# Optimization experiments

Measured on AMD Instinct MI355X. Metric: run time of the kernel, lower is better.

## Reference

```python
import jax, jax.numpy as jnp
import numpy as np
from math import factorial, pi, sqrt

N_ATOMS = 4096
N_PAIRS = 49152
F = 16           # num_tensordense_features
NUM_RADIAL = 16  # basis num=16
NUM_SPECIES = 95
EMB_DIM = 32
CUTOFF = 5.0
LMAX = 4         # SelfAttention max_degree=4
NLM = 25
LMAX_B = 2       # basis max_degree=2 (also max_tensordense_degree)
NLM_B = 9

DEG9 = np.repeat(np.arange(3), [1, 3, 5])        # degree index of each lm, l<=2
DEG25 = np.repeat(np.arange(5), [1, 3, 5, 7, 9]) # degree index of each lm, l<=4


def real_sph(u, lmax):
    # real spherical harmonics (m = -l..l ordering, no Condon-Shortley), u: (...,3) unit vectors
    x, y, z = u[..., 0], u[..., 1], u[..., 2]
    phi = jnp.arctan2(y, x)
    ct = jnp.clip(z, -1.0, 1.0)
    st = jnp.sqrt(jnp.clip(1.0 - ct * ct, 0.0, 1.0))
    P = {(0, 0): jnp.ones_like(ct)}
    for m in range(1, lmax + 1):
        P[(m, m)] = -(2 * m - 1) * st * P[(m - 1, m - 1)]
    for m in range(0, lmax):
        P[(m + 1, m)] = (2 * m + 1) * ct * P[(m, m)]
    for m in range(0, lmax + 1):
        for l in range(m + 2, lmax + 1):
            P[(l, m)] = ((2 * l - 1) * ct * P[(l - 1, m)] - (l + m - 1) * P[(l - 2, m)]) / (l - m)
    outs = []
    for l in range(lmax + 1):
        for m in range(-l, l + 1):
            ma = abs(m)
            Nn = sqrt((2 * l + 1) / (4 * pi) * factorial(l - ma) / factorial(l + ma))
            cs = (-1.0) ** ma  # cancel Condon-Shortley in P
            if m == 0:
                Y = Nn * P[(l, 0)]
            elif m > 0:
                Y = sqrt(2.0) * Nn * cs * jnp.cos(m * phi) * P[(l, m)]
            else:
                Y = sqrt(2.0) * Nn * cs * jnp.sin(ma * phi) * P[(l, ma)]
            outs.append(Y)
    return jnp.stack(outs, axis=-1)


def _gaunt():
    # exact real Gaunt (CG-equivalent) coupling coefficients via Gauss-Legendre x uniform-phi quadrature
    nt, nph = 16, 32
    xs, ws = np.polynomial.legendre.leggauss(nt)
    phis = np.arange(nph) * (2 * np.pi / nph)
    ct = np.repeat(xs, nph); ph = np.tile(phis, nt)
    st = np.sqrt(np.clip(1.0 - ct ** 2, 0.0, 1.0))
    u = np.stack([st * np.cos(ph), st * np.sin(ph), ct], -1)
    w = np.repeat(ws, nph) * (2 * np.pi / nph)
    Y = np.asarray(real_sph(jnp.asarray(u, dtype=jnp.float32), LMAX))
    G = np.einsum('gi,gj,gk,g->ijk', Y, Y[:, :NLM_B], Y, w)
    G[np.abs(G) < 1e-6] = 0.0
    return G

_G = _gaunt()
G_ATT = jnp.asarray(_G, dtype=jnp.float32)                      # (25, 9, 25): feat x basis -> feat
G_TD = jnp.asarray(_G[:NLM_B, :, :NLM_B], dtype=jnp.float32)    # (9, 9, 9): TensorDense coupling


def pdense(x, W, deg):
    return jnp.einsum('plf,lfg->plg', x, W[deg])


def couple(xf, Bf, G):
    # equivariant tensor product  out[p,k,f] = sum_ij G[i,j,k] xf[p,i,f] Bf[p,j,f]
    u = jnp.einsum('pif,ijk->pjkf', xf, G)
    return jnp.einsum('pjf,pjkf->pkf', Bf, u)


def setup_inputs() -> dict:
    key = jax.random.key(0)
    ks = jax.random.split(key, 24)
    s = 1.0 / np.sqrt(F)
    inp = dict(
        atomic_numbers=jax.random.randint(ks[0], (N_ATOMS,), 0, NUM_SPECIES),
        neighbour_indices=jnp.stack([
            jax.random.randint(ks[1], (N_PAIRS,), 0, N_ATOMS),
            jax.random.randint(ks[2], (N_PAIRS,), 0, N_ATOMS)], axis=-1),
        neighbour_displacements=jax.random.normal(ks[3], (N_PAIRS, 3), dtype=jnp.float32) * 1.7,
        W_rad=jax.random.normal(ks[4], (NUM_SPECIES, NUM_RADIAL, F), dtype=jnp.float32) / np.sqrt(NUM_RADIAL),
        emb_table=jax.random.normal(ks[5], (NUM_SPECIES, EMB_DIM), dtype=jnp.float32),
        W_emb=jax.random.normal(ks[6], (EMB_DIM, F), dtype=jnp.float32) / np.sqrt(EMB_DIM),
        b_emb=jnp.zeros((F,), jnp.float32),
        td_W1=jax.random.normal(ks[7], (3, F, F), dtype=jnp.float32) * s,
        td_W2=jax.random.normal(ks[8], (3, F, F), dtype=jnp.float32) * s,
        td_W3=jax.random.normal(ks[9], (3, F, F), dtype=jnp.float32) * s,
        Wb1=jax.random.normal(ks[10], (NUM_RADIAL, F), dtype=jnp.float32) / np.sqrt(NUM_RADIAL),
        Wq1=jax.random.normal(ks[11], (5, F, F), dtype=jnp.float32) * s,
        Wk1=jax.random.normal(ks[12], (5, F, F), dtype=jnp.float32) * s,
        Wv1=jax.random.normal(ks[13], (5, F, F), dtype=jnp.float32) * s,
        Wo1=jax.random.normal(ks[14], (5, F, F), dtype=jnp.float32) * s,
        bo1=jnp.zeros((F,), jnp.float32),
        Wb2=jax.random.normal(ks[15], (NUM_RADIAL, F), dtype=jnp.float32) / np.sqrt(NUM_RADIAL),
        Wq2=jax.random.normal(ks[16], (5, F, F), dtype=jnp.float32) * s,
        Wk2=jax.random.normal(ks[17], (5, F, F), dtype=jnp.float32) * s,
        Wv2=jax.random.normal(ks[18], (5, F, F), dtype=jnp.float32) * s,
        Wo2=jax.random.normal(ks[19], (5, F, F), dtype=jnp.float32) * s,
        bo2=jnp.zeros((F,), jnp.float32),
    )
    return inp


def reference(atomic_numbers, neighbour_indices, neighbour_displacements,
              W_rad, emb_table, W_emb, b_emb, td_W1, td_W2, td_W3,
              Wb1, Wq1, Wk1, Wv1, Wo1, bo1, Wb2, Wq2, Wk2, Wv2, Wo2, bo2):
    dst = neighbour_indices[:, 0]   # idx_i
    src = neighbour_indices[:, 1]   # idx_j
    Zj = atomic_numbers[src]
    r = jnp.linalg.norm(neighbour_displacements, axis=-1)
    u = neighbour_displacements / jnp.maximum(r, 1e-9)[:, None]
    sh = real_sph(u, LMAX)          # (P, 25)
    sh_b = sh[:, :NLM_B]            # (P, 9)
    kk = jnp.arange(1, NUM_RADIAL + 1, dtype=jnp.float32)
    rb = jnp.sinc(kk[None, :] * r[:, None] / CUTOFF) * (r < CUTOFF)[:, None]  # sinc basis w/ cutoff
    # species-aware radial basis -> per-pair equivariant features (P, 9, F)
    y0 = jnp.einsum('pk,pkf->pf', rb, W_rad[Zj])
    y = sh_b[:, :, None] * y0[:, None, :]
    # TensorDense: dense -> CG tensor product -> dense (degrees <= 2)
    a = pdense(y, td_W1, DEG9)
    b = pdense(y, td_W2, DEG9)
    u9 = jnp.einsum('pif,ijk->pjkf', a, G_TD)
    tp = jnp.einsum('pjf,pjkf->pkf', b, u9)
    y = pdense(tp, td_W3, DEG9)
    # aggregate per-pair messages to atoms (segment mean), pad degrees to l<=4
    sums = jnp.zeros((N_ATOMS, NLM_B, F), y.dtype).at[dst].add(y)
    cnt = jnp.zeros((N_ATOMS,), y.dtype).at[dst].add(1.0)
    x = sums / jnp.maximum(cnt, 1.0)[:, None, None]
    x = jnp.pad(x, ((0, 0), (0, NLM - NLM_B), (0, 0)))  # (N, 25, F)
    # two segment self-attention layers over neighbour pairs
    for (Wb, Wq, Wk, Wv, Wo, bo) in ((Wb1, Wq1, Wk1, Wv1, Wo1, bo1), (Wb2, Wq2, Wk2, Wv2, Wo2, bo2)):
        Bf = sh_b[:, :, None] * (rb @ Wb)[:, None, :]   # projected pair basis (P, 9, F)
        q = pdense(x, Wq, DEG25)[dst]
        kf = couple(pdense(x, Wk, DEG25)[src], Bf, G_ATT)
        vf = couple(pdense(x, Wv, DEG25)[src], Bf, G_ATT)
        s = jnp.einsum('plf,plf->p', q, kf) / np.sqrt(NLM * F)
        m = jax.lax.stop_gradient(jnp.full((N_ATOMS,), -1e30, s.dtype).at[dst].max(s))
        e = jnp.exp(s - m[dst])
        den = jnp.zeros((N_ATOMS,), s.dtype).at[dst].add(e)
        alpha = e / (den[dst] + 1e-9)
        agg = jnp.zeros((N_ATOMS, NLM, F), x.dtype).at[dst].add(alpha[:, None, None] * vf)
        x = pdense(agg, Wo, DEG25)
        x = x.at[:, 0, :].add(bo)
    # embedding residual connection on the scalar (l=0) channel
    res = emb_table[atomic_numbers] @ W_emb + b_emb
    x = x.at[:, 0, :].add(res)
    return x
```

## Files before the change

### kernel.cpp

```cpp
#include <hip/hip_runtime.h>
#include <hip/hip_bf16.h>

#define NA 4096
#define NP 49152

typedef _Float16 f16;
typedef _Float16 h2 __attribute__((ext_vector_type(2)));
union U4H { uint4 u; f16 h[8]; h2 p[4]; };

__device__ __forceinline__ float fdot2(h2 a, h2 b, float c){
#if __has_builtin(__builtin_amdgcn_fdot2)
  return __builtin_amdgcn_fdot2(a, b, c, false);
#else
  return c + (float)a.x*(float)b.x + (float)a.y*(float)b.y;
#endif
}

constexpr int WS_AOFS9 = 64;
constexpr int WS_ATTW9 = 128;
constexpr int WS_ATTIJ9= WS_ATTW9 + 512;
constexpr int WS_G     = 12800;
constexpr int WS_NATT  = WS_G + 5632;
constexpr int WS_ATTW  = WS_NATT + 8;
constexpr int WS_ATTIJ = WS_ATTW + 1024;
constexpr int WS_TDOFS = WS_ATTIJ + 1024;
constexpr int WS_TDW   = WS_TDOFS + 16;
constexpr int WS_TDIJ  = WS_TDW + 512;
constexpr int WS_AOFS  = WS_TDIJ + 512;
constexpr int WS_SH    = WS_AOFS + 32;
constexpr int WS_RB    = WS_SH + NP*9;
constexpr int WS_S     = WS_RB + NP*16;
constexpr int WS_CCNT  = WS_S + NP;
constexpr int WS_COFF  = WS_CCNT + NA;
constexpr int WS_CCUR  = WS_COFF + NA + 8;
constexpr int WS_CLST  = WS_CCUR + NA;
constexpr int WS_XQ    = WS_CLST + NP;
constexpr int WS_XK    = WS_XQ + NA*400;
constexpr int WS_XV    = WS_XK + NA*400;
constexpr int WS_PVF   = WS_XV + NA*400;
constexpr int WS_WW    = WS_PVF + NP*128;
constexpr int WS_PVFE  = WS_PVF + NP*256;
constexpr int WS_INV   = WS_PVFE;
constexpr int WS_DS    = WS_INV + NP;
constexpr long long WS_END = (long long)WS_DS + 2*NP + 16;

__device__ const float  GLX[16] = {
  -0.98940093499164993f, -0.94457502307323258f, -0.86563120238783174f, -0.75540440835500303f,
  -0.61787624440264375f, -0.45801677765722739f, -0.28160355077925891f, -0.09501250983763744f,
   0.09501250983763744f,  0.28160355077925891f,  0.45801677765722739f,  0.61787624440264375f,
   0.75540440835500303f,  0.86563120238783174f,  0.94457502307323258f,  0.98940093499164993f };
__device__ const double GLW[16] = {
  0.02715245941175409, 0.06225352393864789, 0.09515851168249278, 0.12462897125553387,
  0.14959598881657673, 0.16915651939500254, 0.18260341504492359, 0.18945061045506850,
  0.18945061045506850, 0.18260341504492359, 0.16915651939500254, 0.14959598881657673,
  0.12462897125553387, 0.09515851168249278, 0.06225352393864789, 0.02715245941175409 };

#define PI_D 3.14159265358979323846

__device__ __forceinline__ float scrub(float v){
  if(!(v == v)) return 0.f;
  return fminf(fmaxf(v, -1e30f), 1e30f);
}

__device__ void real_sph25(float ct, float phi, float* Y){
  float st = sqrtf(fmaxf(0.f, 1.f - ct*ct));
  float P[5][5];
  P[0][0] = 1.f;
  #pragma unroll
  for(int m=1;m<=4;m++) P[m][m] = -(2.f*m - 1.f)*st*P[m-1][m-1];
  #pragma unroll
  for(int m=0;m<4;m++) P[m+1][m] = (2.f*m + 1.f)*ct*P[m][m];
  #pragma unroll
  for(int m=0;m<=4;m++){
    #pragma unroll
    for(int l=m+2;l<=4;l++)
      P[l][m] = ((2.f*l - 1.f)*ct*P[l-1][m] - (float)(l+m-1)*P[l-2][m]) / (float)(l-m);
  }
  const double fact[9] = {1,1,2,6,24,120,720,5040,40320};
  int idx = 0;
  #pragma unroll
  for(int l=0;l<=4;l++){
    #pragma unroll
    for(int m=-l;m<=l;m++){
      int ma = (m < 0) ? -m : m;
      float Nn = (float)sqrt((2*l+1)/(4.0*PI_D)*fact[l-ma]/fact[l+ma]);
      float cs = (ma & 1) ? -1.f : 1.f;
      float v;
      if(m == 0)      v = Nn * P[l][0];
      else if(m > 0)  v = 1.4142135623730951f * Nn * cs * cosf(ma*phi) * P[l][ma];
      else            v = 1.4142135623730951f * Nn * cs * sinf(ma*phi) * P[l][ma];
      Y[idx++] = v;
    }
  }
}

__global__ __launch_bounds__(256) void kq_G(float* ws){
  __shared__ float Ysh[12800];
  int tid = threadIdx.x;
  for(int pt=tid; pt<512; pt+=256){
    float ct  = GLX[pt >> 5];
    float phi = (float)((pt & 31) * (2.0*PI_D/32.0));
    float Y[25];
    real_sph25(ct, phi, Y);
    #pragma unroll
    for(int i=0;i<25;i++) Ysh[pt*25 + i] = Y[i];
  }
  __syncthreads();
  int idx = blockIdx.x*256 + tid;
  int t = idx >> 3, chunk = idx & 7;
  if(t >= 5625) return;
  int k = t % 25, j = (t/25) % 9, i = t/225;
  double acc = 0.0;
  int g0 = chunk*64;
  #pragma unroll 4
  for(int g=g0; g<g0+64; g++){
    double w = GLW[g >> 5] * (2.0*PI_D/32.0);
    acc += w * (double)Ysh[g*25+i] * (double)Ysh[g*25+j] * (double)Ysh[g*25+k];
  }
  acc += __shfl_xor(acc, 1, 8);
  acc += __shfl_xor(acc, 2, 8);
  acc += __shfl_xor(acc, 4, 8);
  if(chunk == 0){
    if(fabs(acc) < 1e-6) acc = 0.0;
    ws[WS_G + (i*9+j)*25 + k] = (float)acc;
  }
}

__global__ __launch_bounds__(64) void kq_lists(float* ws){
  __shared__ float Gsh[5632];
  __shared__ int cA[25], cT[9], cA9[25], oA[26], oT[10], oA9[26];
  int t = threadIdx.x;
  for(int i=t; i<5625; i+=64) Gsh[i] = ws[WS_G + i];
  __syncthreads();
  const float* G = Gsh;
  if(t < 25){
    int c=0, c9=0;
    for(int i=0;i<25;i++) for(int j=0;j<9;j++) if(G[(i*9+j)*25+t] != 0.f){ c++; if(i<9) c9++; }
    cA[t]=c; cA9[t]=c9;
  }
  if(t < 9){  int c=0; for(int i=0;i<9;i++)  for(int j=0;j<9;j++) if(G[(i*9+j)*25+t] != 0.f) c++; cT[t]=c; }
  __syncthreads();
  if(t == 0){
    int s=0; for(int k=0;k<25;k++){ oA[k]=s; s+=cA[k]; } oA[25]=s;
    ((int*)ws)[WS_NATT] = s;
    s=0; for(int k=0;k<25;k++){ oA9[k]=s; s+=cA9[k]; } oA9[25]=s;
    s=0; for(int k=0;k<9;k++){ oT[k]=s; s+=cT[k]; } oT[9]=s;
  }
  __syncthreads();
  float* attw = ws + WS_ATTW;  int* attij = (int*)ws + WS_ATTIJ;
  float* attw9 = ws + WS_ATTW9; int* attij9 = (int*)ws + WS_ATTIJ9;
  int* aofs  = (int*)ws + WS_AOFS;
  int* aofs9 = (int*)ws + WS_AOFS9;
  if(t < 26){ aofs[t] = oA[t] < 1024 ? oA[t] : 1024; aofs9[t] = oA9[t] < 512 ? oA9[t] : 512; }
  if(t < 25){
    int pos = oA[t], pos9 = oA9[t];
    for(int i=0;i<25;i++) for(int j=0;j<9;j++){
      float w = G[(i*9+j)*25+t];
      if(w != 0.f){
        if(pos < 1024){ attw[pos]=w; attij[pos] = i | (j<<5) | (t<<9); pos++; }
        if(i < 9 && pos9 < 512){ attw9[pos9]=w; attij9[pos9] = i | (j<<5) | (t<<9); pos9++; }
      }
    }
  }
  float* tdw = ws + WS_TDW; int* tdij = (int*)ws + WS_TDIJ; int* tdofs = (int*)ws + WS_TDOFS;
  if(t < 9){
    int pos = oT[t];
    for(int i=0;i<9;i++) for(int j=0;j<9;j++){
      float w = G[(i*9+j)*25+t];
      if(w != 0.f && pos < 512){
        int li = (i==0)?0:(i<4)?1:2, lj = (j==0)?0:(j<4)?1:2;
        tdw[pos]=w; tdij[pos] = i | (j<<5) | (li<<10) | (lj<<12); pos++;
      }
    }
    tdofs[t] = oT[t];
    if(t == 0) tdofs[9] = oT[9];
  }
}

__global__ void k_cnt(const int* nbr, float* ws){
  int p = blockIdx.x*256 + threadIdx.x;
  if(p >= NP) return;
  atomicAdd((int*)ws + WS_CCNT + nbr[2*p], 1);
}

__global__ __launch_bounds__(1024) void k_scan(float* ws){
  __shared__ int part[1024];
  int t = threadIdx.x;
  const int* cnt = (const int*)ws + WS_CCNT;
  int v0 = cnt[4*t], v1 = cnt[4*t+1], v2 = cnt[4*t+2], v3 = cnt[4*t+3];
  part[t] = v0+v1+v2+v3;
  __syncthreads();
  for(int o=1; o<1024; o<<=1){
    int x = (t >= o) ? part[t-o] : 0;
    __syncthreads();
    part[t] += x;
    __syncthreads();
  }
  int base = (t > 0) ? part[t-1] : 0;
  int* offp = (int*)ws + WS_COFF;
  int* cur  = (int*)ws + WS_CCUR;
  offp[4*t]   = base;          cur[4*t]   = base;
  offp[4*t+1] = base+v0;       cur[4*t+1] = base+v0;
  offp[4*t+2] = base+v0+v1;    cur[4*t+2] = base+v0+v1;
  offp[4*t+3] = base+v0+v1+v2; cur[4*t+3] = base+v0+v1+v2;
  if(t == 1023) offp[4096] = part[1023];
}

__global__ void k_fill(const int* nbr, float* ws){
  int p = blockIdx.x*256 + threadIdx.x;
  if(p >= NP) return;
  int d = nbr[2*p], s = nbr[2*p+1];
  int pos = atomicAdd((int*)ws + WS_CCUR + d, 1);
  ((int*)ws)[WS_CLST + pos] = p;
  ((int*)ws)[WS_INV + p] = pos;
  ((int*)ws)[WS_DS + 2*pos]     = d;
  ((int*)ws)[WS_DS + 2*pos + 1] = s;
}

__global__ void k_pair(const float* disp, float* ws){
  int p = blockIdx.x*256 + threadIdx.x;
  if(p >= NP) return;
  int sp = ((const int*)ws)[WS_INV + p];
  float dx = disp[3*p], dy = disp[3*p+1], dz = disp[3*p+2];
  float r = sqrtf(dx*dx + dy*dy + dz*dz);
  float inv = 1.f / fmaxf(r, 1e-9f);
  float ux = dx*inv, uy = dy*inv, uz = dz*inv;
  float sh[9];
  sh[0] = 0.28209479177387814f;
  sh[1] = 0.4886025119029199f * uy;
  sh[2] = 0.4886025119029199f * uz;
  sh[3] = 0.4886025119029199f * ux;
  sh[4] = 1.0925484305920792f * ux*uy;
  sh[5] = 1.0925484305920792f * uy*uz;
  sh[6] = 0.31539156525252005f * (3.f*uz*uz - 1.f);
  sh[7] = 1.0925484305920792f * ux*uz;
  sh[8] = 0.5462742152960396f * (ux*ux - uy*uy);
  #pragma unroll
  for(int i=0;i<9;i++) ws[WS_SH + sp*9 + i] = scrub(sh[i]);
  float mask = (r < 5.f) ? 1.f : 0.f;
  float rbv[16];
  #pragma unroll
  for(int k=1;k<=16;k++){
    float x  = (float)k * r * 0.2f;
    float px = 3.14159265358979323846f * x;
    float s  = (px < 1e-6f) ? 1.f : (sinf(px)/px);
    rbv[k-1] = scrub(s * mask);
  }
  float4* rb4 = (float4*)(ws + WS_RB + sp*16);
  #pragma unroll
  for(int c=0;c<4;c++) rb4[c] = make_float4(rbv[4*c], rbv[4*c+1], rbv[4*c+2], rbv[4*c+3]);
}

__global__ __launch_bounds__(256) void k_ww(const float* Wrad, const float* W1,
                                            const float* W2, float* ws){
  int s = blockIdx.x;
  #pragma unroll
  for(int it=0; it<6; it++){
    int idx = threadIdx.x + 256*it;
    int w = idx / 768, r = idx % 768;
    int d = r / 256, r2 = r % 256, k = r2 / 16, g = r2 % 16;
    const float* Wsrc = (w == 0) ? W1 : W2;
    float acc = 0.f;
    #pragma unroll
    for(int fp=0; fp<16; fp++)
      acc += Wrad[(s*16+k)*16+fp] * Wsrc[(d*16+fp)*16+g];
    ws[WS_WW + ((size_t)(s*2+w)*16 + g)*48 + d*16 + k] = acc;
  }
}

__global__ __launch_bounds__(256) void k_td(const int* aZ, const float* W3, float* ws){
  __shared__ float sh_s[16][9];
  __shared__ float S_s[16][88];
  __shared__ float tp_s[16][9][16];
  int tid = threadIdx.x, pl = tid >> 4, g = tid & 15;
  int sp = blockIdx.x*16 + pl;
  int src = ((const int*)ws)[WS_DS + 2*sp + 1];
  int Zj = aZ[src];
  {
    float4* S4 = (float4*)&S_s[0][0];
    for(int t0=tid; t0<352; t0+=256) S4[t0] = make_float4(0.f,0.f,0.f,0.f);
  }
  if(g < 9) sh_s[pl][g] = ws[WS_SH + sp*9 + g];
  float rb[16];
  {
    const float4* rb4 = (const float4*)(ws + WS_RB + sp*16);
    #pragma unroll
    for(int c=0;c<4;c++){
      float4 r = rb4[c];
      rb[4*c]=r.x; rb[4*c+1]=r.y; rb[4*c+2]=r.z; rb[4*c+3]=r.w;
    }
  }
  float A1[3], A2[3];
  {
    const float4* w1 = (const float4*)(ws + WS_WW + ((size_t)(Zj*2+0)*16+g)*48);
    const float4* w2 = (const float4*)(ws + WS_WW + ((size_t)(Zj*2+1)*16+g)*48);
    #pragma unroll
    for(int d=0; d<3; d++){
      float a1 = 0.f, a2 = 0.f;
      #pragma unroll
      for(int c=0;c<4;c++){
        float4 x1 = w1[d*4+c], x2 = w2[d*4+c];
        a1 += x1.x*rb[4*c] + x1.y*rb[4*c+1] + x1.z*rb[4*c+2] + x1.w*rb[4*c+3];
        a2 += x2.x*rb[4*c] + x2.y*rb[4*c+1] + x2.z*rb[4*c+2] + x2.w*rb[4*c+3];
      }
      A1[d] = a1; A2[d] = a2;
    }
  }
  __syncthreads();
  if(g < 9){
    const float* tdw = ws + WS_TDW;
    const int* tdij  = (const int*)ws + WS_TDIJ;
    const int* tdofs = (const int*)ws + WS_TDOFS;
    int e1 = tdofs[g+1];
    for(int e=tdofs[g]; e<e1; e++){
      float w = tdw[e]; int meta = tdij[e];
      int i = meta & 31, j = (meta>>5) & 15, li = (meta>>10) & 3, lj = (meta>>12) & 3;
      S_s[pl][g*9 + li*3 + lj] += w * sh_s[pl][i] * sh_s[pl][j];
    }
  }
  __syncthreads();
  float AA[9];
  #pragma unroll
  for(int li=0;li<3;li++)
    #pragma unroll
    for(int lj=0;lj<3;lj++) AA[li*3+lj] = A1[li]*A2[lj];
  #pragma unroll
  for(int k=0;k<9;k++){
    float tpv = 0.f;
    #pragma unroll
    for(int c=0;c<9;c++) tpv += S_s[pl][k*9+c] * AA[c];
    tp_s[pl][k][g] = tpv;
  }
  __syncthreads();
  float w3r[48];
  #pragma unroll
  for(int d=0;d<3;d++)
    #pragma unroll
    for(int f2=0;f2<16;f2++) w3r[d*16+f2] = W3[(d*16+f2)*16+g];
  float acc9[9];
  #pragma unroll
  for(int k=0;k<9;k++){
    int d = (k==0)?0:(k<4)?1:2;
    const float4* t4 = (const float4*)&tp_s[pl][k][0];
    float acc = 0.f;
    #pragma unroll
    for(int c=0;c<4;c++){
      float4 t = t4[c];
      acc += t.x*w3r[d*16+4*c] + t.y*w3r[d*16+4*c+1] + t.z*w3r[d*16+4*c+2] + t.w*w3r[d*16+4*c+3];
    }
    acc9[k] = scrub(acc);
  }
  f16* ptd = (f16*)(ws + WS_PVF) + (size_t)sp*256 + g*16;
  U4H u0, u1;
  #pragma unroll
  for(int j=0;j<8;j++) u0.h[j] = (f16)acc9[j];
  u1.h[0] = (f16)acc9[8];
  #pragma unroll
  for(int j=1;j<8;j++) u1.h[j] = (f16)0.f;
  *(uint4*)(ptd)     = u0.u;
  *(uint4*)(ptd + 8) = u1.u;
}

__global__ __launch_bounds__(256) void k_tdq(const float* Wq, const float* Wk,
                                             const float* Wv, float* ws){
  __shared__ float xsh[4][144];
  __shared__ float wq_sh[768], wk_sh[768], wv_sh[768];
  int tid = threadIdx.x, al = tid >> 6, lane = tid & 63;
  int a = blockIdx.x*4 + al;
  for(int t=tid; t<768; t+=256){ wq_sh[t]=Wq[t]; wk_sh[t]=Wk[t]; wv_sh[t]=Wv[t]; }
  const int* coff = (const int*)ws + WS_COFF;
  int off0 = coff[a], n = coff[a+1] - off0;
  const f16* base = (const f16*)(ws + WS_PVF);
  float acc[8] = {0,0,0,0,0,0,0,0};
  if(lane < 32){
    for(int t=0; t<n; t++){
      U4H u; u.u = *(const uint4*)(base + (size_t)(off0+t)*256 + lane*8);
      #pragma unroll
      for(int j=0;j<8;j++) acc[j] += (float)u.h[j];
    }
  }
  float invn = 1.f / fmaxf((float)n, 1.f);
  if(lane < 32){
    int gg = lane >> 1;
    #pragma unroll
    for(int j=0;j<8;j++){
      int k = (lane & 1)*8 + j;
      if(k < 9) xsh[al][k*16 + gg] = scrub(acc[j]*invn);
    }
  }
  __syncthreads();
  int g = lane & 15, q4 = lane >> 4;
  f16* qt = (f16*)(ws + WS_XQ) + (size_t)a*800 + g*32;
  f16* kt = (f16*)(ws + WS_XK) + (size_t)a*800 + g*32;
  f16* vt = (f16*)(ws + WS_XV) + (size_t)a*800 + g*32;
  for(int i=q4; i<9; i+=4){
    int l = (i==0)?0:(i<4)?1:2;
    float q=0.f, k2=0.f, v2=0.f;
    #pragma unroll
    for(int f2=0;f2<16;f2++){
      float xv = xsh[al][i*16+f2];
      q  += xv*wq_sh[(l*16+f2)*16+g];
      k2 += xv*wk_sh[(l*16+f2)*16+g];
      v2 += xv*wv_sh[(l*16+f2)*16+g];
    }
    qt[i] = (f16)q; kt[i] = (f16)k2; vt[i] = (f16)v2;
  }
}

template<int NI>
__global__ __launch_bounds__(128) void k_att(const float* Wb, float* ws){
  constexpr int MROWH = (NI == 9) ? 16 : 32;
  constexpr int PLSTR = (NI == 9) ? 408 : 840;
  __shared__ __align__(16) f16 Ml[8][PLSTR];
  __shared__ float sh_s[8][9];
  __shared__ float wb_sh[256];
  constexpr int NPAIR = NI/2;
  constexpr int TAIL  = NI-1;
  int tid = threadIdx.x, pl = tid >> 4, g = tid & 15;
  int sp = blockIdx.x*8 + pl;
  {
    uint4 z; z.x=0; z.y=0; z.z=0; z.w=0;
    uint4* Mz = (uint4*)&Ml[0][0];
    for(int t0=tid; t0<PLSTR; t0+=128) Mz[t0] = z;
  }
  for(int t0=tid; t0<256; t0+=128) wb_sh[t0] = Wb[t0];
  if(g < 9) sh_s[pl][g] = ws[WS_SH + sp*9 + g];
  __syncthreads();
  {
    const float* attw = ws + (NI==9 ? WS_ATTW9 : WS_ATTW);
    const int* attij  = (const int*)ws + (NI==9 ? WS_ATTIJ9 : WS_ATTIJ);
    const int* aofs   = (const int*)ws + (NI==9 ? WS_AOFS9 : WS_AOFS);
    for(int kr=g; kr<25; kr+=16){
      f16* Mrow = &Ml[pl][kr*MROWH];
      int e = aofs[kr], e1 = aofs[kr+1];
      if(e < e1){
        int meta = attij[e];
        int curi = meta & 31;
        float cur = 0.f;
        for(; e<e1; e++){
          meta = attij[e];
          int i2 = meta & 31;
          if(i2 != curi){ Mrow[curi] = (f16)cur; cur = 0.f; curi = i2; }
          cur += attw[e] * sh_s[pl][(meta>>5) & 15];
        }
        Mrow[curi] = (f16)cur;
      }
    }
  }
  __syncthreads();
  int dst = ((const int*)ws)[WS_DS + 2*sp];
  int src = ((const int*)ws)[WS_DS + 2*sp + 1];
  float q_r[NI];
  {
    const f16* qt = (const f16*)(ws + WS_XQ) + (size_t)dst*800 + g*32;
    #pragma unroll
    for(int c=0;c<NPAIR/4;c++){
      U4H u; u.u = *(const uint4*)(qt + c*8);
      #pragma unroll
      for(int j=0;j<8;j++) q_r[c*8+j] = (float)u.h[j];
    }
    q_r[TAIL] = (float)qt[TAIL];
  }
  h2 xk2[NPAIR], xv2[NPAIR];
  float xkT, xvT;
  {
    const f16* kt = (const f16*)(ws + WS_XK) + (size_t)src*800 + g*32;
    const f16* vt = (const f16*)(ws + WS_XV) + (size_t)src*800 + g*32;
    #pragma unroll
    for(int c=0;c<NPAIR/4;c++){
      U4H uk; uk.u = *(const uint4*)(kt + c*8);
      U4H uv; uv.u = *(const uint4*)(vt + c*8);
      #pragma unroll
      for(int j=0;j<4;j++){ xk2[c*4+j] = uk.p[j]; xv2[c*4+j] = uv.p[j]; }
    }
    xkT = (float)kt[TAIL];
    xvT = (float)vt[TAIL];
  }
  float wbf;
  {
    const float4* rb4 = (const float4*)(ws + WS_RB + sp*16);
    float acc = 0.f;
    #pragma unroll
    for(int c=0;c<4;c++){
      float4 r = rb4[c];
      acc += r.x*wb_sh[(4*c)*16+g] + r.y*wb_sh[(4*c+1)*16+g]
           + r.z*wb_sh[(4*c+2)*16+g] + r.w*wb_sh[(4*c+3)*16+g];
    }
    wbf = acc;
  }
  f16* pvf = (f16*)(ws + WS_PVF) + (size_t)sp*400;
  float sacc = 0.f;
  #pragma unroll
  for(int k=0;k<25;k++){
    const uint4* Mq = (const uint4*)&Ml[pl][k*MROWH];
    float mT = (float)Ml[pl][k*MROWH + TAIL];
    float vv = 0.f, kf = 0.f;
    #pragma unroll
    for(int c=0;c<NPAIR/4;c++){
      U4H u; u.u = Mq[c];
      #pragma unroll
      for(int j=0;j<4;j++){
        vv = fdot2(u.p[j], xv2[c*4+j], vv);
        if(k < NI) kf = fdot2(u.p[j], xk2[c*4+j], kf);
      }
    }
    vv += mT * xvT;
    if(k < NI){
      kf += mT * xkT;
      sacc += q_r[k]*kf;
    }
    pvf[k*16 + g] = (f16)scrub(wbf*vv);
  }
  float sl = sacc;
  #pragma unroll
  for(int off=1; off<16; off<<=1) sl += __shfl_xor(sl, off, 16);
  if(g == 0) ws[WS_S + sp] = scrub(sl * 0.05f);
}

template<bool FINAL>
__global__ __launch_bounds__(256) void k_aggo(const float* Wo, const float* bo,
    const int* aZ, const float* emb, const float* Wemb, const float* bemb,
    const float* Wq, const float* Wk, const float* Wv, float* ws, float* out){
  __shared__ float xsh[4][400];
  __shared__ float wo_sh[1280];
  __shared__ float wq_sh[FINAL?4:1280], wk_sh[FINAL?4:1280], wv_sh[FINAL?4:1280];
  __shared__ float osh[FINAL?4:1600];
  int tid = threadIdx.x, al = tid >> 6, lane = tid & 63;
  int a = blockIdx.x*4 + al;
  for(int t=tid; t<1280; t+=256){
    wo_sh[t] = Wo[t];
    if(!FINAL){ wq_sh[t]=Wq[t]; wk_sh[t]=Wk[t]; wv_sh[t]=Wv[t]; }
  }
  const int* coff = (const int*)ws + WS_COFF;
  int off0 = coff[a], n = coff[a+1] - off0;
  float mx = -1e30f;
  for(int t=lane; t<n; t+=64) mx = fmaxf(mx, ws[WS_S + off0 + t]);
  #pragma unroll
  for(int off=1; off<64; off<<=1) mx = fmaxf(mx, __shfl_xor(mx, off));
  float den = 0.f;
  for(int t=lane; t<n; t+=64) den += expf(fminf(ws[WS_S + off0 + t] - mx, 0.f));
  #pragma unroll
  for(int off=1; off<64; off<<=1) den += __shfl_xor(den, off);
  float inv_den = 1.f / (den + 1e-9f);
  float acc[8] = {0,0,0,0,0,0,0,0};
  const f16* base = (const f16*)(ws + WS_PVF);
  for(int t=0; t<n; t++){
    float alpha = expf(fminf(ws[WS_S + off0 + t] - mx, 0.f)) * inv_den;
    if(lane < 50){
      U4H u; u.u = *(const uint4*)(base + (size_t)(off0+t)*400 + lane*8);
      #pragma unroll
      for(int j=0;j<8;j++) acc[j] += alpha * (float)u.h[j];
    }
  }
  if(lane < 50){
    #pragma unroll
    for(int j=0;j<8;j++) xsh[al][lane*8 + j] = scrub(acc[j]);
  }
  __syncthreads();
  int g = lane & 15, q4 = lane >> 4;
  for(int i=q4; i<25; i+=4){
    int l = (i==0)?0:(i<4)?1:(i<9)?2:(i<16)?3:4;
    float accv = 0.f;
    #pragma unroll
    for(int f2=0;f2<16;f2++) accv += xsh[al][i*16+f2]*wo_sh[(l*16+f2)*16+g];
    if(i == 0){
      accv += bo[g];
      if(FINAL){
        int Z = aZ[a];
        float res = bemb[g];
        #pragma unroll
        for(int e2=0;e2<32;e2++) res += emb[Z*32+e2]*Wemb[e2*16+g];
        accv += res;
      }
    }
    if(FINAL) out[a*400 + i*16 + g] = scrub(accv);
    else      osh[al*400 + i*16 + g] = scrub(accv);
  }
  if(!FINAL){
    __syncthreads();
    f16* qt = (f16*)(ws + WS_XQ) + (size_t)a*800 + g*32;
    f16* kt = (f16*)(ws + WS_XK) + (size_t)a*800 + g*32;
    f16* vt = (f16*)(ws + WS_XV) + (size_t)a*800 + g*32;
    for(int i=q4; i<25; i+=4){
      int l = (i==0)?0:(i<4)?1:(i<9)?2:(i<16)?3:4;
      float q=0.f, k2=0.f, v2=0.f;
      #pragma unroll
      for(int f2=0;f2<16;f2++){
        float xv = osh[al*400 + i*16 + f2];
        q  += xv*wq_sh[(l*16+f2)*16+g];
        k2 += xv*wk_sh[(l*16+f2)*16+g];
        v2 += xv*wv_sh[(l*16+f2)*16+g];
      }
      qt[i] = (f16)q; kt[i] = (f16)k2; vt[i] = (f16)v2;
    }
  }
}

extern "C" void kernel_launch(void* const* d_in, const int* in_sizes, int n_in,
                              void* d_out, int out_size, void* d_ws, size_t ws_size,
                              hipStream_t stream){
  (void)in_sizes; (void)n_in; (void)out_size;
  if(ws_size < (size_t)WS_END * sizeof(float)) return;
  float* ws = (float*)d_ws;
  const int* aZ  = (const int*)d_in[0];
  const int* nbr = (const int*)d_in[1];
  const float* disp = (const float*)d_in[2];
  const float* Wrad = (const float*)d_in[3];
  const float* emb  = (const float*)d_in[4];
  const float* Wemb = (const float*)d_in[5];
  const float* bemb = (const float*)d_in[6];
  const float* W1   = (const float*)d_in[7];
  const float* W2   = (const float*)d_in[8];
  const float* W3   = (const float*)d_in[9];
  const float* Wb1 = (const float*)d_in[10]; const float* Wq1 = (const float*)d_in[11];
  const float* Wk1 = (const float*)d_in[12]; const float* Wv1 = (const float*)d_in[13];
  const float* Wo1 = (const float*)d_in[14]; const float* bo1 = (const float*)d_in[15];
  const float* Wb2 = (const float*)d_in[16]; const float* Wq2 = (const float*)d_in[17];
  const float* Wk2 = (const float*)d_in[18]; const float* Wv2 = (const float*)d_in[19];
  const float* Wo2 = (const float*)d_in[20]; const float* bo2 = (const float*)d_in[21];

  kq_G<<<176,256,0,stream>>>(ws);
  kq_lists<<<1,64,0,stream>>>(ws);
  hipMemsetAsync(ws + WS_CCNT, 0, NA*sizeof(int), stream);
  k_cnt<<<192,256,0,stream>>>(nbr, ws);
  k_scan<<<1,1024,0,stream>>>(ws);
  k_fill<<<192,256,0,stream>>>(nbr, ws);
  k_pair<<<192,256,0,stream>>>(disp, ws);
  k_ww<<<95,256,0,stream>>>(Wrad, W1, W2, ws);
  k_td<<<3072,256,0,stream>>>(aZ, W3, ws);
  k_tdq<<<1024,256,0,stream>>>(Wq1, Wk1, Wv1, ws);

  k_att<9><<<6144,128,0,stream>>>(Wb1, ws);
  k_aggo<false><<<1024,256,0,stream>>>(Wo1, bo1, aZ, emb, Wemb, bemb,
                                       Wq2, Wk2, Wv2, ws, nullptr);
  k_att<25><<<6144,128,0,stream>>>(Wb2, ws);
  k_aggo<true><<<1024,256,0,stream>>>(Wo2, bo2, aZ, emb, Wemb, bemb,
                                      nullptr, nullptr, nullptr, ws, (float*)d_out);
}
```

Baseline: 400.1 us.

## Merge setup kernels into two launches and split fdot2 accumulator chains

The separate setup launches are merged into two block-partitioned kernels: Gaunt, weight-product and neighbour-count in one, and list build, CSR fill and pair features in the other. Pair features are now written directly at the sorted slot, so the inverse-permutation buffer and its extra gather disappear. In the attention kernel the fdot2 reductions use two independent accumulators to shorten dependency chains. This removes several launches and a pass over the pairs, at the cost of putting unrelated work in the same grid and slightly reordering the floating-point summation.

```diff
diff --git a/kernel.cpp b/kernel.cpp
--- a/kernel.cpp
+++ b/kernel.cpp
@@ -40,8 +40,7 @@
 constexpr int WS_PVF   = WS_XV + NA*400;
 constexpr int WS_WW    = WS_PVF + NP*128;
 constexpr int WS_PVFE  = WS_PVF + NP*256;
-constexpr int WS_INV   = WS_PVFE;
-constexpr int WS_DS    = WS_INV + NP;
+constexpr int WS_DS    = WS_PVFE;
 constexpr long long WS_END = (long long)WS_DS + 2*NP + 16;
 
 __device__ const float  GLX[16] = {
@@ -94,93 +93,56 @@
   }
 }
 
-__global__ __launch_bounds__(256) void kq_G(float* ws){
+__global__ __launch_bounds__(256) void k_u1(const float* Wrad, const float* W1,
+    const float* W2, const int* nbr, float* ws){
   __shared__ float Ysh[12800];
-  int tid = threadIdx.x;
-  for(int pt=tid; pt<512; pt+=256){
-    float ct  = GLX[pt >> 5];
-    float phi = (float)((pt & 31) * (2.0*PI_D/32.0));
-    float Y[25];
-    real_sph25(ct, phi, Y);
-    #pragma unroll
-    for(int i=0;i<25;i++) Ysh[pt*25 + i] = Y[i];
-  }
-  __syncthreads();
-  int idx = blockIdx.x*256 + tid;
-  int t = idx >> 3, chunk = idx & 7;
-  if(t >= 5625) return;
-  int k = t % 25, j = (t/25) % 9, i = t/225;
-  double acc = 0.0;
-  int g0 = chunk*64;
-  #pragma unroll 4
-  for(int g=g0; g<g0+64; g++){
-    double w = GLW[g >> 5] * (2.0*PI_D/32.0);
-    acc += w * (double)Ysh[g*25+i] * (double)Ysh[g*25+j] * (double)Ysh[g*25+k];
-  }
-  acc += __shfl_xor(acc, 1, 8);
-  acc += __shfl_xor(acc, 2, 8);
-  acc += __shfl_xor(acc, 4, 8);
-  if(chunk == 0){
-    if(fabs(acc) < 1e-6) acc = 0.0;
-    ws[WS_G + (i*9+j)*25 + k] = (float)acc;
-  }
-}
-
-__global__ __launch_bounds__(64) void kq_lists(float* ws){
-  __shared__ float Gsh[5632];
-  __shared__ int cA[25], cT[9], cA9[25], oA[26], oT[10], oA9[26];
-  int t = threadIdx.x;
-  for(int i=t; i<5625; i+=64) Gsh[i] = ws[WS_G + i];
-  __syncthreads();
-  const float* G = Gsh;
-  if(t < 25){
-    int c=0, c9=0;
-    for(int i=0;i<25;i++) for(int j=0;j<9;j++) if(G[(i*9+j)*25+t] != 0.f){ c++; if(i<9) c9++; }
-    cA[t]=c; cA9[t]=c9;
-  }
-  if(t < 9){  int c=0; for(int i=0;i<9;i++)  for(int j=0;j<9;j++) if(G[(i*9+j)*25+t] != 0.f) c++; cT[t]=c; }
-  __syncthreads();
-  if(t == 0){
-    int s=0; for(int k=0;k<25;k++){ oA[k]=s; s+=cA[k]; } oA[25]=s;
-    ((int*)ws)[WS_NATT] = s;
-    s=0; for(int k=0;k<25;k++){ oA9[k]=s; s+=cA9[k]; } oA9[25]=s;
-    s=0; for(int k=0;k<9;k++){ oT[k]=s; s+=cT[k]; } oT[9]=s;
-  }
-  __syncthreads();
-  float* attw = ws + WS_ATTW;  int* attij = (int*)ws + WS_ATTIJ;
-  float* attw9 = ws + WS_ATTW9; int* attij9 = (int*)ws + WS_ATTIJ9;
-  int* aofs  = (int*)ws + WS_AOFS;
-  int* aofs9 = (int*)ws + WS_AOFS9;
-  if(t < 26){ aofs[t] = oA[t] < 1024 ? oA[t] : 1024; aofs9[t] = oA9[t] < 512 ? oA9[t] : 512; }
-  if(t < 25){
-    int pos = oA[t], pos9 = oA9[t];
-    for(int i=0;i<25;i++) for(int j=0;j<9;j++){
-      float w = G[(i*9+j)*25+t];
-      if(w != 0.f){
-        if(pos < 1024){ attw[pos]=w; attij[pos] = i | (j<<5) | (t<<9); pos++; }
-        if(i < 9 && pos9 < 512){ attw9[pos9]=w; attij9[pos9] = i | (j<<5) | (t<<9); pos9++; }
-      }
-    }
-  }
-  float* tdw = ws + WS_TDW; int* tdij = (int*)ws + WS_TDIJ; int* tdofs = (int*)ws + WS_TDOFS;
-  if(t < 9){
-    int pos = oT[t];
-    for(int i=0;i<9;i++) for(int j=0;j<9;j++){
-      float w = G[(i*9+j)*25+t];
-      if(w != 0.f && pos < 512){
-        int li = (i==0)?0:(i<4)?1:2, lj = (j==0)?0:(j<4)?1:2;
-        tdw[pos]=w; tdij[pos] = i | (j<<5) | (li<<10) | (lj<<12); pos++;
-      }
-    }
-    tdofs[t] = oT[t];
-    if(t == 0) tdofs[9] = oT[9];
-  }
-}
-
-__global__ void k_cnt(const int* nbr, float* ws){
-  int p = blockIdx.x*256 + threadIdx.x;
-  if(p >= NP) return;
-  atomicAdd((int*)ws + WS_CCNT + nbr[2*p], 1);
+  int b = blockIdx.x, tid = threadIdx.x;
+  if(b < 176){
+    for(int pt=tid; pt<512; pt+=256){
+      float ct  = GLX[pt >> 5];
+      float phi = (float)((pt & 31) * (2.0*PI_D/32.0));
+      float Y[25];
+      real_sph25(ct, phi, Y);
+      #pragma unroll
+      for(int i=0;i<25;i++) Ysh[pt*25 + i] = Y[i];
+    }
+    __syncthreads();
+    int idx = b*256 + tid;
+    int t = idx >> 3, chunk = idx & 7;
+    if(t >= 5625) return;
+    int k = t % 25, j = (t/25) % 9, i = t/225;
+    double acc = 0.0;
+    int g0 = chunk*64;
+    #pragma unroll 4
+    for(int g=g0; g<g0+64; g++){
+      double w = GLW[g >> 5] * (2.0*PI_D/32.0);
+      acc += w * (double)Ysh[g*25+i] * (double)Ysh[g*25+j] * (double)Ysh[g*25+k];
+    }
+    acc += __shfl_xor(acc, 1, 8);
+    acc += __shfl_xor(acc, 2, 8);
+    acc += __shfl_xor(acc, 4, 8);
+    if(chunk == 0){
+      if(fabs(acc) < 1e-6) acc = 0.0;
+      ws[WS_G + (i*9+j)*25 + k] = (float)acc;
+    }
+  } else if(b < 271){
+    int s = b - 176;
+    #pragma unroll
+    for(int it=0; it<6; it++){
+      int idx = tid + 256*it;
+      int w = idx / 768, r = idx % 768;
+      int d = r / 256, r2 = r % 256, k = r2 / 16, g = r2 % 16;
+      const float* Wsrc = (w == 0) ? W1 : W2;
+      float acc = 0.f;
+      #pragma unroll
+      for(int fp=0; fp<16; fp++)
+        acc += Wrad[(s*16+k)*16+fp] * Wsrc[(d*16+fp)*16+g];
+      ws[WS_WW + ((size_t)(s*2+w)*16 + g)*48 + d*16 + k] = acc;
+    }
+  } else {
+    int p = (b-271)*256 + tid;
+    if(p < NP) atomicAdd((int*)ws + WS_CCNT + nbr[2*p], 1);
+  }
 }
 
 __global__ __launch_bounds__(1024) void k_scan(float* ws){
@@ -206,65 +168,91 @@
   if(t == 1023) offp[4096] = part[1023];
 }
 
-__global__ void k_fill(const int* nbr, float* ws){
-  int p = blockIdx.x*256 + threadIdx.x;
-  if(p >= NP) return;
-  int d = nbr[2*p], s = nbr[2*p+1];
-  int pos = atomicAdd((int*)ws + WS_CCUR + d, 1);
-  ((int*)ws)[WS_CLST + pos] = p;
-  ((int*)ws)[WS_INV + p] = pos;
-  ((int*)ws)[WS_DS + 2*pos]     = d;
-  ((int*)ws)[WS_DS + 2*pos + 1] = s;
-}
-
-__global__ void k_pair(const float* disp, float* ws){
-  int p = blockIdx.x*256 + threadIdx.x;
-  if(p >= NP) return;
-  int sp = ((const int*)ws)[WS_INV + p];
-  float dx = disp[3*p], dy = disp[3*p+1], dz = disp[3*p+2];
-  float r = sqrtf(dx*dx + dy*dy + dz*dz);
-  float inv = 1.f / fmaxf(r, 1e-9f);
-  float ux = dx*inv, uy = dy*inv, uz = dz*inv;
-  float sh[9];
-  sh[0] = 0.28209479177387814f;
-  sh[1] = 0.4886025119029199f * uy;
-  sh[2] = 0.4886025119029199f * uz;
-  sh[3] = 0.4886025119029199f * ux;
-  sh[4] = 1.0925484305920792f * ux*uy;
-  sh[5] = 1.0925484305920792f * uy*uz;
-  sh[6] = 0.31539156525252005f * (3.f*uz*uz - 1.f);
-  sh[7] = 1.0925484305920792f * ux*uz;
-  sh[8] = 0.5462742152960396f * (ux*ux - uy*uy);
-  #pragma unroll
-  for(int i=0;i<9;i++) ws[WS_SH + sp*9 + i] = scrub(sh[i]);
-  float mask = (r < 5.f) ? 1.f : 0.f;
-  float rbv[16];
-  #pragma unroll
-  for(int k=1;k<=16;k++){
-    float x  = (float)k * r * 0.2f;
-    float px = 3.14159265358979323846f * x;
-    float s  = (px < 1e-6f) ? 1.f : (sinf(px)/px);
-    rbv[k-1] = scrub(s * mask);
-  }
-  float4* rb4 = (float4*)(ws + WS_RB + sp*16);
-  #pragma unroll
-  for(int c=0;c<4;c++) rb4[c] = make_float4(rbv[4*c], rbv[4*c+1], rbv[4*c+2], rbv[4*c+3]);
-}
-
-__global__ __launch_bounds__(256) void k_ww(const float* Wrad, const float* W1,
-                                            const float* W2, float* ws){
-  int s = blockIdx.x;
-  #pragma unroll
-  for(int it=0; it<6; it++){
-    int idx = threadIdx.x + 256*it;
-    int w = idx / 768, r = idx % 768;
-    int d = r / 256, r2 = r % 256, k = r2 / 16, g = r2 % 16;
-    const float* Wsrc = (w == 0) ? W1 : W2;
-    float acc = 0.f;
-    #pragma unroll
-    for(int fp=0; fp<16; fp++)
-      acc += Wrad[(s*16+k)*16+fp] * Wsrc[(d*16+fp)*16+g];
-    ws[WS_WW + ((size_t)(s*2+w)*16 + g)*48 + d*16 + k] = acc;
+__global__ __launch_bounds__(256) void k_u2(const float* disp, const int* nbr, float* ws){
+  __shared__ float Gsh[5632];
+  __shared__ int cA[25], cT[9], cA9[25], oA[26], oT[10], oA9[26];
+  if(blockIdx.x == 0){
+    int t = threadIdx.x;
+    for(int i=t; i<5625; i+=256) Gsh[i] = ws[WS_G + i];
+    __syncthreads();
+    const float* G = Gsh;
+    if(t < 25){
+      int c=0, c9=0;
+      for(int i=0;i<25;i++) for(int j=0;j<9;j++) if(G[(i*9+j)*25+t] != 0.f){ c++; if(i<9) c9++; }
+      cA[t]=c; cA9[t]=c9;
+    }
+    if(t < 9){ int c=0; for(int i=0;i<9;i++) for(int j=0;j<9;j++) if(G[(i*9+j)*25+t] != 0.f) c++; cT[t]=c; }
+    __syncthreads();
+    if(t == 0){
+      int s=0; for(int k=0;k<25;k++){ oA[k]=s; s+=cA[k]; } oA[25]=s;
+      ((int*)ws)[WS_NATT] = s;
+      s=0; for(int k=0;k<25;k++){ oA9[k]=s; s+=cA9[k]; } oA9[25]=s;
+      s=0; for(int k=0;k<9;k++){ oT[k]=s; s+=cT[k]; } oT[9]=s;
+    }
+    __syncthreads();
+    float* attw = ws + WS_ATTW;  int* attij = (int*)ws + WS_ATTIJ;
+    float* attw9 = ws + WS_ATTW9; int* attij9 = (int*)ws + WS_ATTIJ9;
+    int* aofs  = (int*)ws + WS_AOFS;
+    int* aofs9 = (int*)ws + WS_AOFS9;
+    if(t < 26){ aofs[t] = oA[t] < 1024 ? oA[t] : 1024; aofs9[t] = oA9[t] < 512 ? oA9[t] : 512; }
+    if(t < 25){
+      int pos = oA[t], pos9 = oA9[t];
+      for(int i=0;i<25;i++) for(int j=0;j<9;j++){
+        float w = G[(i*9+j)*25+t];
+        if(w != 0.f){
+          if(pos < 1024){ attw[pos]=w; attij[pos] = i | (j<<5) | (t<<9); pos++; }
+          if(i < 9 && pos9 < 512){ attw9[pos9]=w; attij9[pos9] = i | (j<<5) | (t<<9); pos9++; }
+        }
+      }
+    }
+    float* tdw = ws + WS_TDW; int* tdij = (int*)ws + WS_TDIJ; int* tdofs = (int*)ws + WS_TDOFS;
+    if(t < 9){
+      int pos = oT[t];
+      for(int i=0;i<9;i++) for(int j=0;j<9;j++){
+        float w = G[(i*9+j)*25+t];
+        if(w != 0.f && pos < 512){
+          int li = (i==0)?0:(i<4)?1:2, lj = (j==0)?0:(j<4)?1:2;
+          tdw[pos]=w; tdij[pos] = i | (j<<5) | (li<<10) | (lj<<12); pos++;
+        }
+      }
+      tdofs[t] = oT[t];
+      if(t == 0) tdofs[9] = oT[9];
+    }
+  } else {
+    int p = (blockIdx.x-1)*256 + threadIdx.x;
+    if(p >= NP) return;
+    int d = nbr[2*p], s = nbr[2*p+1];
+    int sp = atomicAdd((int*)ws + WS_CCUR + d, 1);
+    ((int*)ws)[WS_DS + 2*sp]     = d;
+    ((int*)ws)[WS_DS + 2*sp + 1] = s;
+    float dx = disp[3*p], dy = disp[3*p+1], dz = disp[3*p+2];
+    float r = sqrtf(dx*dx + dy*dy + dz*dz);
+    float inv = 1.f / fmaxf(r, 1e-9f);
+    float ux = dx*inv, uy = dy*inv, uz = dz*inv;
+    float sh[9];
+    sh[0] = 0.28209479177387814f;
+    sh[1] = 0.4886025119029199f * uy;
+    sh[2] = 0.4886025119029199f * uz;
+    sh[3] = 0.4886025119029199f * ux;
+    sh[4] = 1.0925484305920792f * ux*uy;
+    sh[5] = 1.0925484305920792f * uy*uz;
+    sh[6] = 0.31539156525252005f * (3.f*uz*uz - 1.f);
+    sh[7] = 1.0925484305920792f * ux*uz;
+    sh[8] = 0.5462742152960396f * (ux*ux - uy*uy);
+    #pragma unroll
+    for(int i=0;i<9;i++) ws[WS_SH + sp*9 + i] = scrub(sh[i]);
+    float mask = (r < 5.f) ? 1.f : 0.f;
+    float rbv[16];
+    #pragma unroll
+    for(int k=1;k<=16;k++){
+      float x  = (float)k * r * 0.2f;
+      float px = 3.14159265358979323846f * x;
+      float s2 = (px < 1e-6f) ? 1.f : (sinf(px)/px);
+      rbv[k-1] = scrub(s2 * mask);
+    }
+    float4* rb4 = (float4*)(ws + WS_RB + sp*16);
+    #pragma unroll
+    for(int c=0;c<4;c++) rb4[c] = make_float4(rbv[4*c], rbv[4*c+1], rbv[4*c+2], rbv[4*c+3]);
   }
 }
 
@@ -494,19 +482,24 @@
   for(int k=0;k<25;k++){
     const uint4* Mq = (const uint4*)&Ml[pl][k*MROWH];
     float mT = (float)Ml[pl][k*MROWH + TAIL];
-    float vv = 0.f, kf = 0.f;
+    float vv0 = 0.f, vv1 = 0.f, kf0 = 0.f, kf1 = 0.f;
     #pragma unroll
     for(int c=0;c<NPAIR/4;c++){
       U4H u; u.u = Mq[c];
-      #pragma unroll
-      for(int j=0;j<4;j++){
-        vv = fdot2(u.p[j], xv2[c*4+j], vv);
-        if(k < NI) kf = fdot2(u.p[j], xk2[c*4+j], kf);
+      vv0 = fdot2(u.p[0], xv2[c*4+0], vv0);
+      vv1 = fdot2(u.p[1], xv2[c*4+1], vv1);
+      vv0 = fdot2(u.p[2], xv2[c*4+2], vv0);
+      vv1 = fdot2(u.p[3], xv2[c*4+3], vv1);
+      if(k < NI){
+        kf0 = fdot2(u.p[0], xk2[c*4+0], kf0);
+        kf1 = fdot2(u.p[1], xk2[c*4+1], kf1);
+        kf0 = fdot2(u.p[2], xk2[c*4+2], kf0);
+        kf1 = fdot2(u.p[3], xk2[c*4+3], kf1);
       }
     }
-    vv += mT * xvT;
+    float vv = vv0 + vv1 + mT*xvT;
     if(k < NI){
-      kf += mT * xkT;
+      float kf = kf0 + kf1 + mT*xkT;
       sacc += q_r[k]*kf;
     }
     pvf[k*16 + g] = (f16)scrub(wbf*vv);
@@ -619,14 +612,10 @@
   const float* Wk2 = (const float*)d_in[18]; const float* Wv2 = (const float*)d_in[19];
   const float* Wo2 = (const float*)d_in[20]; const float* bo2 = (const float*)d_in[21];
 
-  kq_G<<<176,256,0,stream>>>(ws);
-  kq_lists<<<1,64,0,stream>>>(ws);
   hipMemsetAsync(ws + WS_CCNT, 0, NA*sizeof(int), stream);
-  k_cnt<<<192,256,0,stream>>>(nbr, ws);
+  k_u1<<<463,256,0,stream>>>(Wrad, W1, W2, nbr, ws);
   k_scan<<<1,1024,0,stream>>>(ws);
-  k_fill<<<192,256,0,stream>>>(nbr, ws);
-  k_pair<<<192,256,0,stream>>>(disp, ws);
-  k_ww<<<95,256,0,stream>>>(Wrad, W1, W2, ws);
+  k_u2<<<193,256,0,stream>>>(disp, nbr, ws);
   k_td<<<3072,256,0,stream>>>(aZ, W3, ws);
   k_tdq<<<1024,256,0,stream>>>(Wq1, Wk1, Wv1, ws);
 
```

Result: faster. 390.3 us (-2.4%).
